# Kernel tuning notes

Hardware: AMD Instinct MI355X
Metric: run time of the kernel (lower is better)

Reference implementation:

```python
import jax, jax.numpy as jnp
import numpy as np

EMBED = 256
NH = 8
NL = 3
NP = 4
HD = EMBED // NH
P2 = 2 * NP  # left+right sampling points are concatenated along the point axis
SHAPES = [(100, 100), (50, 50), (25, 25)]


def setup_inputs() -> dict:
    key = jax.random.key(0)
    ks = jax.random.split(key, 10)
    b, nq, nk = 4, 300, 17
    lq = nq * nk
    L = sum(h * w for h, w in SHAPES)

    def lin(k, o, i):
        return jax.random.normal(k, (o, i), jnp.float32) / np.float32(np.sqrt(i))

    return {
        "query": jax.random.normal(ks[0], (b, lq, EMBED), jnp.float32),
        "reference_points_l": jax.random.uniform(ks[1], (b, nq, NL, nk, 2), jnp.float32),
        "reference_points_r": jax.random.uniform(ks[2], (b, nq, NL, nk, 2), jnp.float32),
        "value": jax.random.normal(ks[3], (b, L, EMBED * 2), jnp.float32),
        "value_spatial_shapes": jnp.array(SHAPES, jnp.int32),
        "value_mask": jnp.zeros((b, L), bool),
        "W_off": lin(ks[4], NH * NL * NP * 4, EMBED),
        "b_off": jax.random.normal(ks[5], (NH * NL * NP * 4,), jnp.float32) * 0.01,
        "W_attn": lin(ks[6], NH * NL * NP, EMBED),
        "b_attn": jnp.zeros((NH * NL * NP,), jnp.float32),
        "W_val": lin(ks[7], EMBED, EMBED * 2),
        "b_val": jnp.zeros((EMBED,), jnp.float32),
        "W_out": lin(ks[8], EMBED, EMBED),
        "b_out": jnp.zeros((EMBED,), jnp.float32),
    }


def _bilinear_sample(v_flat, locs, H, W):
    # v_flat: [b, nh, H*W, hd]; locs: [b, nh, lq, P, 2] normalized to [0,1].
    # Matches torch grid_sample(bilinear, padding=zeros, align_corners=False)
    # with grid = 2*loc - 1  =>  pixel coord = loc*size - 0.5.
    x = locs[..., 0] * W - 0.5
    y = locs[..., 1] * H - 0.5
    x0 = jnp.floor(x)
    y0 = jnp.floor(y)
    tx = x - x0
    ty = y - y0
    x0i = x0.astype(jnp.int32)
    y0i = y0.astype(jnp.int32)
    b, nh, lq, P = x.shape
    out = jnp.zeros(x.shape + (v_flat.shape[-1],), v_flat.dtype)
    for dy, wy in ((0, 1.0 - ty), (1, ty)):
        for dx, wx in ((0, 1.0 - tx), (1, tx)):
            xi = x0i + dx
            yi = y0i + dy
            valid = (xi >= 0) & (xi < W) & (yi >= 0) & (yi < H)
            idx = jnp.clip(yi, 0, H - 1) * W + jnp.clip(xi, 0, W - 1)
            g = jnp.take_along_axis(
                v_flat, idx.reshape(b, nh, lq * P, 1), axis=2
            ).reshape(b, nh, lq, P, -1)
            out = out + (wx * wy * valid.astype(v_flat.dtype))[..., None] * g
    return out


def reference(query, reference_points_l, reference_points_r, value,
              value_spatial_shapes, value_mask,
              W_off, b_off, W_attn, b_attn, W_val, b_val, W_out, b_out):
    shapes = np.asarray(value_spatial_shapes)  # static level shapes
    b, lq, _ = query.shape

    # value projection + padding mask (True -> zero, matching masked_fill)
    v = value @ W_val.T + b_val
    v = jnp.where(value_mask[..., None], jnp.zeros((), v.dtype), v)
    v = v.reshape(b, -1, NH, HD)

    off = (query @ W_off.T + b_off).reshape(b, lq, NH, NL, NP, 4)
    aw = (query @ W_attn.T + b_attn).reshape(b, lq, NH, NL * NP)
    aw = jax.nn.softmax(aw, axis=-1).reshape(b, lq, NH, NL, NP)

    # rearrange 'b nq nl nk s -> b (nq nk) nl s'
    rl = jnp.transpose(reference_points_l, (0, 1, 3, 2, 4)).reshape(b, lq, NL, 2)
    rr = jnp.transpose(reference_points_r, (0, 1, 3, 2, 4)).reshape(b, lq, NL, 2)

    # offset normalizer: (W, H) per level
    norm = jnp.stack([value_spatial_shapes[:, 1], value_spatial_shapes[:, 0]], -1).astype(query.dtype)
    locs_l = rl[:, :, None, :, None, :] + off[..., :2] / norm[None, None, None, :, None, :]
    locs_r = rr[:, :, None, :, None, :] + off[..., 2:] / norm[None, None, None, :, None, :]
    locs = jnp.concatenate([locs_l, locs_r], axis=-2)  # [b,lq,nh,nl,P2,2]
    w = jnp.concatenate([aw, aw], axis=-1)             # [b,lq,nh,nl,P2]

    out = jnp.zeros((b, NH, lq, HD), query.dtype)
    start = 0
    for l in range(NL):
        H, W = int(shapes[l, 0]), int(shapes[l, 1])
        v_l = jnp.transpose(v[:, start:start + H * W], (0, 2, 1, 3))  # [b,nh,HW,hd]
        locs_lvl = jnp.transpose(locs[:, :, :, l], (0, 2, 1, 3, 4))   # [b,nh,lq,P2,2]
        samp = _bilinear_sample(v_l, locs_lvl, H, W)                  # [b,nh,lq,P2,hd]
        w_lvl = jnp.transpose(w[:, :, :, l], (0, 2, 1, 3))            # [b,nh,lq,P2]
        out = out + jnp.einsum('bnqp,bnqpd->bnqd', w_lvl, samp)
        start += H * W

    out = jnp.transpose(out, (0, 2, 1, 3)).reshape(b, lq, EMBED)
    return out @ W_out.T + b_out
```

## Files before the change

### kernel.cpp

```cpp
#include <hip/hip_runtime.h>

#define NH    8
#define NLVL  3
#define HD    32
#define EMBED 256

constexpr int LTOT = 13125;
constexpr int BQ   = 4;
constexpr int NQ   = 300;
constexpr int NK   = 17;
constexpr int LQ   = NQ * NK;
constexpr int MV   = BQ * LTOT;
constexpr int MQ   = BQ * LQ;

typedef _Float16 f16x8 __attribute__((ext_vector_type(8)));
typedef _Float16 f16x4 __attribute__((ext_vector_type(4)));
typedef float    f32x4 __attribute__((ext_vector_type(4)));

constexpr int CW_WV   = 32768;
constexpr int CW_WOFF = CW_WV   + 24576;
constexpr int CW_WAT  = CW_WOFF + 6144;
constexpr int CW_TOT  = CW_WAT  + 16384;

__global__ __launch_bounds__(256)
void convert_w(const float* __restrict__ Wval, const float* __restrict__ Woff,
               const float* __restrict__ Wattn, const float* __restrict__ Wout,
               const float* __restrict__ boff, const float* __restrict__ battn,
               _Float16* __restrict__ Wv16, _Float16* __restrict__ Wqc16,
               _Float16* __restrict__ Wo16, float* __restrict__ bqc)
{
    const int idx = blockIdx.x * 256 + threadIdx.x;
    if (idx < 480) bqc[idx] = (idx < 384) ? boff[idx] : battn[idx - 384];
    if (idx >= CW_TOT) return;

    const float* src; _Float16* dst; size_t e;
    if      (idx < CW_WV)   { src = Wval;  dst = Wv16;          e = (size_t)idx * 4; }
    else if (idx < CW_WOFF) { src = Woff;  dst = Wqc16;         e = (size_t)(idx - CW_WV) * 4; }
    else if (idx < CW_WAT)  { src = Wattn; dst = Wqc16 + 98304; e = (size_t)(idx - CW_WOFF) * 4; }
    else                    { src = Wout;  dst = Wo16;          e = (size_t)(idx - CW_WAT) * 4; }

    const float4 x = *reinterpret_cast<const float4*>(src + e);
    f16x4 o;
    o[0] = (_Float16)x.x; o[1] = (_Float16)x.y;
    o[2] = (_Float16)x.z; o[3] = (_Float16)x.w;
    *reinterpret_cast<f16x4*>(dst + e) = o;
}

template<bool AF16, int OUT>
__global__ __launch_bounds__(256)
void gemm_f16(const float* __restrict__ A32, const _Float16* __restrict__ A16,
              const _Float16* __restrict__ Bg,
              const float* __restrict__ bias,
              float* __restrict__ Cf, _Float16* __restrict__ Ch,
              int M, int N, int K, const unsigned char* __restrict__ rowmask)
{
    __shared__ _Float16 Ah[2][4096], Bh[2][4096];

    const int tid  = threadIdx.x;
    const int lane = tid & 63;
    const int w    = tid >> 6;
    const int wr   = w >> 1, wc = w & 1;
    const int row0 = blockIdx.y * 128;
    const int col0 = blockIdx.x * 128;
    const int nt   = K >> 5;

    int cr[2], ck[2];
#pragma unroll
    for (int s = 0; s < 2; ++s) {
        const int i = tid + s * 256;
        cr[s] = ((i >> 6) << 4) + (i & 15);
        ck[s] = ((i >> 4) & 3) << 3;
    }

    float4 a32r[2][2];
    uint4  a16r[2], bhr[2];

    auto issue = [&](int kt) {
        const int kk = kt << 5;
#pragma unroll
        for (int s = 0; s < 2; ++s) {
            const int ga = row0 + cr[s];
            const size_t ao = (size_t)ga * K + kk + ck[s];
            if constexpr (AF16) {
                if (ga < M) a16r[s] = *reinterpret_cast<const uint4*>(A16 + ao);
                else        a16r[s] = make_uint4(0, 0, 0, 0);
            } else {
                if (ga < M) {
                    a32r[s][0] = *reinterpret_cast<const float4*>(A32 + ao);
                    a32r[s][1] = *reinterpret_cast<const float4*>(A32 + ao + 4);
                } else {
                    a32r[s][0] = make_float4(0.f, 0.f, 0.f, 0.f);
                    a32r[s][1] = make_float4(0.f, 0.f, 0.f, 0.f);
                }
            }
            const int gb = col0 + cr[s];
            if (gb < N)
                bhr[s] = *reinterpret_cast<const uint4*>(Bg + (size_t)gb * K + kk + ck[s]);
            else
                bhr[s] = make_uint4(0, 0, 0, 0);
        }
    };
    auto commit = [&](int buf) {
#pragma unroll
        for (int s = 0; s < 2; ++s) {
            const int i = tid + s * 256;
            if constexpr (AF16) {
                *reinterpret_cast<uint4*>(&Ah[buf][i * 8]) = a16r[s];
            } else {
                float x[8] = {a32r[s][0].x, a32r[s][0].y, a32r[s][0].z, a32r[s][0].w,
                              a32r[s][1].x, a32r[s][1].y, a32r[s][1].z, a32r[s][1].w};
                f16x8 h;
#pragma unroll
                for (int e = 0; e < 8; ++e) h[e] = (_Float16)x[e];
                ((f16x8*)Ah[buf])[i] = h;
            }
            *reinterpret_cast<uint4*>(&Bh[buf][i * 8]) = bhr[s];
        }
    };

    f32x4 acc[4][4];
#pragma unroll
    for (int i = 0; i < 4; ++i)
#pragma unroll
        for (int j = 0; j < 4; ++j) acc[i][j] = (f32x4)(0.f);

    issue(0);
    commit(0);
    __syncthreads();

    int cur = 0;
    for (int t = 0; t < nt; ++t) {
        const bool more = (t + 1 < nt);
        if (more) issue(t + 1);

        f16x8 af[4], bf[4];
#pragma unroll
        for (int ii = 0; ii < 4; ++ii) {
            af[ii] = ((f16x8*)Ah[cur])[(wr * 4 + ii) * 64 + lane];
            bf[ii] = ((f16x8*)Bh[cur])[(wc * 4 + ii) * 64 + lane];
        }
#pragma unroll
        for (int ii = 0; ii < 4; ++ii)
#pragma unroll
            for (int jj = 0; jj < 4; ++jj)
                acc[ii][jj] = __builtin_amdgcn_mfma_f32_16x16x32_f16(af[ii], bf[jj], acc[ii][jj], 0, 0, 0);

        if (more) {
            commit(cur ^ 1);
            __syncthreads();
        }
        cur ^= 1;
    }

    const int rbase = row0 + wr * 64 + (lane >> 4) * 4;
    const int cbase = col0 + wc * 64 + (lane & 15);
#pragma unroll
    for (int jj = 0; jj < 4; ++jj) {
        const int col = cbase + jj * 16;
        if (col >= N) continue;
        const float bv = bias[col];
#pragma unroll
        for (int ii = 0; ii < 4; ++ii)
#pragma unroll
            for (int r4 = 0; r4 < 4; ++r4) {
                const int row = rbase + ii * 16 + r4;
                if (row >= M) continue;
                float val = acc[ii][jj][r4] + bv;
                if constexpr (OUT == 1) {
                    if (rowmask[row]) val = 0.f;
                    const unsigned br = (unsigned)row / 13125u;
                    const int      lr = row - (int)br * 13125;
                    const int      hh = col >> 5, ch = col & 31;
                    Ch[(((size_t)br * NH + hh) * LTOT + lr) * 32 + ch] = (_Float16)val;
                } else if constexpr (OUT == 2) {
                    Ch[(size_t)row * N + col] = (_Float16)val;
                } else {
                    Cf[(size_t)row * N + col] = val;
                }
            }
    }
}

__global__ __launch_bounds__(256)
void msda_sample(const _Float16* __restrict__ v,
                 const _Float16* __restrict__ qo,
                 const float* __restrict__ refl,
                 const float* __restrict__ refr,
                 _Float16* __restrict__ out_pre)
{
    const int g   = threadIdx.x >> 6;
    const int t   = threadIdx.x & 63;
    const int bq  = blockIdx.x * 4 + g;
    const int b   = bq / LQ;
    const int lqi = bq - b * LQ;
    const int iq  = lqi / NK;
    const int ik  = lqi - iq * NK;

    __shared__ float s_off[4][384];
    __shared__ float s_aw[4][96];
    __shared__ float s_ref[4][NLVL][4];

    {
        const _Float16* qop = qo + (size_t)bq * 480;
        for (int i = t; i < 384; i += 64) s_off[g][i] = (float)qop[i];
        for (int i = t; i < 96;  i += 64) s_aw[g][i]  = (float)qop[384 + i];
        if (t < 12) {
            const int nl = t >> 2, comp = t & 3;
            const float* rp = (comp < 2) ? refl : refr;
            s_ref[g][nl][comp] =
                rp[((((size_t)b * NQ + iq) * NLVL + nl) * NK + ik) * 2 + (comp & 1)];
        }
    }
    __syncthreads();

    const int h  = t >> 3;
    const int c4 = (t & 7) * 4;

    float w12[12];
    float mx = -1e30f;
#pragma unroll
    for (int i = 0; i < 12; ++i) { w12[i] = s_aw[g][h * 12 + i]; mx = fmaxf(mx, w12[i]); }
    float sum = 0.f;
#pragma unroll
    for (int i = 0; i < 12; ++i) { w12[i] = __expf(w12[i] - mx); sum += w12[i]; }
    const float inv = 1.f / sum;

    const int   Ls[3]   = {100, 50, 25};
    const int   st[3]   = {0, 10000, 12500};
    const float invN[3] = {0.01f, 0.02f, 0.04f};

    float4 acc = make_float4(0.f, 0.f, 0.f, 0.f);
    const _Float16* vb = v + ((size_t)(b * NH + h) * LTOT) * 32 + c4;

#pragma unroll
    for (int nl = 0; nl < 3; ++nl) {
        const int   Wl = Ls[nl], Hl = Ls[nl];
        const float fS = (float)Wl;
        const int   base = st[nl];
#pragma unroll
        for (int p2 = 0; p2 < 8; ++p2) {
            const int p  = p2 & 3;
            const int rs = (p2 >> 2) & 1;
            const int ob = ((h * 3 + nl) * 4 + p) * 4 + rs * 2;
            const float ox = s_off[g][ob], oy = s_off[g][ob + 1];
            const float rx = s_ref[g][nl][rs * 2], ry = s_ref[g][nl][rs * 2 + 1];
            const float x = (rx + ox * invN[nl]) * fS - 0.5f;
            const float y = (ry + oy * invN[nl]) * fS - 0.5f;
            const float x0 = floorf(x), y0 = floorf(y);
            const float tx = x - x0,   ty = y - y0;
            const int ix = (int)x0, iy = (int)y0;
            const float aww = w12[nl * 4 + p] * inv;

            const int x0c = min(max(ix, 0), Wl - 1);
            const int x1c = min(max(ix + 1, 0), Wl - 1);
            const int y0c = min(max(iy, 0), Hl - 1);
            const int y1c = min(max(iy + 1, 0), Hl - 1);
            const float vx0 = (ix     >= 0 && ix     < Wl) ? 1.f : 0.f;
            const float vx1 = (ix + 1 >= 0 && ix + 1 < Wl) ? 1.f : 0.f;
            const float vy0 = (iy     >= 0 && iy     < Hl) ? 1.f : 0.f;
            const float vy1 = (iy + 1 >= 0 && iy + 1 < Hl) ? 1.f : 0.f;

            const float w00 = (1.f - tx) * (1.f - ty) * vx0 * vy0 * aww;
            const float w10 = tx         * (1.f - ty) * vx1 * vy0 * aww;
            const float w01 = (1.f - tx) * ty         * vx0 * vy1 * aww;
            const float w11 = tx         * ty         * vx1 * vy1 * aww;

            const f16x4 g00 = *reinterpret_cast<const f16x4*>(vb + (size_t)(base + y0c * Wl + x0c) * 32);
            const f16x4 g10 = *reinterpret_cast<const f16x4*>(vb + (size_t)(base + y0c * Wl + x1c) * 32);
            const f16x4 g01 = *reinterpret_cast<const f16x4*>(vb + (size_t)(base + y1c * Wl + x0c) * 32);
            const f16x4 g11 = *reinterpret_cast<const f16x4*>(vb + (size_t)(base + y1c * Wl + x1c) * 32);

            acc.x = fmaf(w00, (float)g00[0], fmaf(w10, (float)g10[0], fmaf(w01, (float)g01[0], fmaf(w11, (float)g11[0], acc.x))));
            acc.y = fmaf(w00, (float)g00[1], fmaf(w10, (float)g10[1], fmaf(w01, (float)g01[1], fmaf(w11, (float)g11[1], acc.y))));
            acc.z = fmaf(w00, (float)g00[2], fmaf(w10, (float)g10[2], fmaf(w01, (float)g01[2], fmaf(w11, (float)g11[2], acc.z))));
            acc.w = fmaf(w00, (float)g00[3], fmaf(w10, (float)g10[3], fmaf(w01, (float)g01[3], fmaf(w11, (float)g11[3], acc.w))));
        }
    }

    f16x4 o;
    o[0] = (_Float16)acc.x; o[1] = (_Float16)acc.y;
    o[2] = (_Float16)acc.z; o[3] = (_Float16)acc.w;
    *reinterpret_cast<f16x4*>(out_pre + (size_t)bq * EMBED + h * HD + c4) = o;
}

extern "C" void kernel_launch(void* const* d_in, const int* in_sizes, int n_in,
                              void* d_out, int out_size, void* d_ws, size_t ws_size,
                              hipStream_t stream)
{
    const float* query  = (const float*)d_in[0];
    const float* refl   = (const float*)d_in[1];
    const float* refr   = (const float*)d_in[2];
    const float* value  = (const float*)d_in[3];
    const unsigned char* vmask = (const unsigned char*)d_in[5];
    const float* W_off  = (const float*)d_in[6];
    const float* b_off  = (const float*)d_in[7];
    const float* W_attn = (const float*)d_in[8];
    const float* b_attn = (const float*)d_in[9];
    const float* W_val  = (const float*)d_in[10];
    const float* b_val  = (const float*)d_in[11];
    const float* W_out  = (const float*)d_in[12];
    const float* b_out  = (const float*)d_in[13];

    char* p = (char*)d_ws;
    _Float16* v      = (_Float16*)p;  p += (size_t)MV * 256 * 2;
    _Float16* qo     = (_Float16*)p;  p += (size_t)MQ * 480 * 2;
    _Float16* outp   = (_Float16*)p;  p += (size_t)MQ * 256 * 2;
    _Float16* Wv16   = (_Float16*)p;  p += 131072 * 2;
    _Float16* Wqc16  = (_Float16*)p;  p += 122880 * 2;
    _Float16* Wo16   = (_Float16*)p;  p += 65536 * 2;
    float* bqc       = (float*)p;     p += 480 * 4;

    convert_w<<<dim3((CW_TOT + 255) / 256), 256, 0, stream>>>(
        W_val, W_off, W_attn, W_out, b_off, b_attn, Wv16, Wqc16, Wo16, bqc);

    gemm_f16<false, 1><<<dim3(2, (MV + 127) / 128), 256, 0, stream>>>(
        value, nullptr, Wv16, b_val, nullptr, v, MV, 256, 512, vmask);

    gemm_f16<false, 2><<<dim3(4, (MQ + 127) / 128), 256, 0, stream>>>(
        query, nullptr, Wqc16, bqc, nullptr, qo, MQ, 480, 256, nullptr);

    msda_sample<<<dim3(MQ / 4), 256, 0, stream>>>(v, qo, refl, refr, outp);

    gemm_f16<true, 0><<<dim3(2, (MQ + 127) / 128), 256, 0, stream>>>(
        nullptr, outp, Wo16, b_out, (float*)d_out, nullptr, MQ, 256, 256, nullptr);
}
```

Baseline: 383.0 us.

## Fuse value/query GEMMs, remap sampler blocks per XCD, precompute sampling metadata

Merges the value and query projection GEMMs into one launch and changes both GEMM kernels to 512-thread blocks where each wave holds a smaller accumulator tile. The sampling kernel maps blocks so each batch's work lands on a fixed pair of XCDs, improving L2 reuse of that batch's value tensor. It also computes the softmax and bilinear corner indices and weights once per point cooperatively into shared memory, instead of redundantly in every thread. The cost is extra shared memory and barriers in the sampler, plus idle padding blocks.

```diff
diff --git a/kernel.cpp b/kernel.cpp
--- a/kernel.cpp
+++ b/kernel.cpp
@@ -12,6 +12,10 @@
 constexpr int LQ   = NQ * NK;
 constexpr int MV   = BQ * LTOT;
 constexpr int MQ   = BQ * LQ;
+
+constexpr int NBLK_V  = 822;
+constexpr int NBLK_QC = 640;
+constexpr int QBPB    = 1275;
 
 typedef _Float16 f16x8 __attribute__((ext_vector_type(8)));
 typedef _Float16 f16x4 __attribute__((ext_vector_type(4)));
@@ -46,13 +50,12 @@
     *reinterpret_cast<f16x4*>(dst + e) = o;
 }
 
-template<bool AF16, int OUT>
-__global__ __launch_bounds__(256)
-void gemm_f16(const float* __restrict__ A32, const _Float16* __restrict__ A16,
-              const _Float16* __restrict__ Bg,
-              const float* __restrict__ bias,
-              float* __restrict__ Cf, _Float16* __restrict__ Ch,
-              int M, int N, int K, const unsigned char* __restrict__ rowmask)
+__global__ __launch_bounds__(512)
+void gemm_vq(const float* __restrict__ value, const _Float16* __restrict__ Wv,
+             const float* __restrict__ bval, _Float16* __restrict__ vout,
+             const unsigned char* __restrict__ vmask,
+             const float* __restrict__ query, const _Float16* __restrict__ Wqc,
+             const float* __restrict__ bqcv, _Float16* __restrict__ qo)
 {
     __shared__ _Float16 Ah[2][4096], Bh[2][4096];
 
@@ -60,67 +63,58 @@
     const int lane = tid & 63;
     const int w    = tid >> 6;
     const int wr   = w >> 1, wc = w & 1;
-    const int row0 = blockIdx.y * 128;
-    const int col0 = blockIdx.x * 128;
-    const int nt   = K >> 5;
-
-    int cr[2], ck[2];
-#pragma unroll
-    for (int s = 0; s < 2; ++s) {
-        const int i = tid + s * 256;
-        cr[s] = ((i >> 6) << 4) + (i & 15);
-        ck[s] = ((i >> 4) & 3) << 3;
-    }
-
-    float4 a32r[2][2];
-    uint4  a16r[2], bhr[2];
+
+    const int  bid = blockIdx.x;
+    const bool isV = bid < NBLK_V;
+    const float* A; const _Float16* Bg; const float* bias;
+    int M, N, K, row0, col0;
+    if (isV) {
+        A = value; Bg = Wv; bias = bval;
+        M = MV; N = 256; K = 512;
+        col0 = (bid & 1) << 7; row0 = (bid >> 1) << 7;
+    } else {
+        const int b2 = bid - NBLK_V;
+        A = query; Bg = Wqc; bias = bqcv;
+        M = MQ; N = 480; K = 256;
+        col0 = (b2 & 3) << 7; row0 = (b2 >> 2) << 7;
+    }
+    const int nt = K >> 5;
+
+    const int cr = ((tid >> 6) << 4) + (tid & 15);
+    const int ck = ((tid >> 4) & 3) << 3;
+
+    float4 a0, a1; uint4 brg;
 
     auto issue = [&](int kt) {
         const int kk = kt << 5;
-#pragma unroll
-        for (int s = 0; s < 2; ++s) {
-            const int ga = row0 + cr[s];
-            const size_t ao = (size_t)ga * K + kk + ck[s];
-            if constexpr (AF16) {
-                if (ga < M) a16r[s] = *reinterpret_cast<const uint4*>(A16 + ao);
-                else        a16r[s] = make_uint4(0, 0, 0, 0);
-            } else {
-                if (ga < M) {
-                    a32r[s][0] = *reinterpret_cast<const float4*>(A32 + ao);
-                    a32r[s][1] = *reinterpret_cast<const float4*>(A32 + ao + 4);
-                } else {
-                    a32r[s][0] = make_float4(0.f, 0.f, 0.f, 0.f);
-                    a32r[s][1] = make_float4(0.f, 0.f, 0.f, 0.f);
-                }
-            }
-            const int gb = col0 + cr[s];
-            if (gb < N)
-                bhr[s] = *reinterpret_cast<const uint4*>(Bg + (size_t)gb * K + kk + ck[s]);
-            else
-                bhr[s] = make_uint4(0, 0, 0, 0);
+        const int ga = row0 + cr;
+        if (ga < M) {
+            const float* ap = A + (size_t)ga * K + kk + ck;
+            a0 = *reinterpret_cast<const float4*>(ap);
+            a1 = *reinterpret_cast<const float4*>(ap + 4);
+        } else {
+            a0 = make_float4(0.f, 0.f, 0.f, 0.f);
+            a1 = make_float4(0.f, 0.f, 0.f, 0.f);
         }
+        const int gb = col0 + cr;
+        if (gb < N)
+            brg = *reinterpret_cast<const uint4*>(Bg + (size_t)gb * K + kk + ck);
+        else
+            brg = make_uint4(0, 0, 0, 0);
     };
     auto commit = [&](int buf) {
-#pragma unroll
-        for (int s = 0; s < 2; ++s) {
-            const int i = tid + s * 256;
-            if constexpr (AF16) {
-                *reinterpret_cast<uint4*>(&Ah[buf][i * 8]) = a16r[s];
-            } else {
-                float x[8] = {a32r[s][0].x, a32r[s][0].y, a32r[s][0].z, a32r[s][0].w,
-                              a32r[s][1].x, a32r[s][1].y, a32r[s][1].z, a32r[s][1].w};
-                f16x8 h;
-#pragma unroll
-                for (int e = 0; e < 8; ++e) h[e] = (_Float16)x[e];
-                ((f16x8*)Ah[buf])[i] = h;
-            }
-            *reinterpret_cast<uint4*>(&Bh[buf][i * 8]) = bhr[s];
-        }
+        f16x8 h;
+        h[0] = (_Float16)a0.x; h[1] = (_Float16)a0.y;
+        h[2] = (_Float16)a0.z; h[3] = (_Float16)a0.w;
+        h[4] = (_Float16)a1.x; h[5] = (_Float16)a1.y;
+        h[6] = (_Float16)a1.z; h[7] = (_Float16)a1.w;
+        ((f16x8*)Ah[buf])[tid] = h;
+        *reinterpret_cast<uint4*>(&Bh[buf][tid * 8]) = brg;
     };
 
-    f32x4 acc[4][4];
-#pragma unroll
-    for (int i = 0; i < 4; ++i)
+    f32x4 acc[2][4];
+#pragma unroll
+    for (int i = 0; i < 2; ++i)
 #pragma unroll
         for (int j = 0; j < 4; ++j) acc[i][j] = (f32x4)(0.f);
 
@@ -133,14 +127,16 @@
         const bool more = (t + 1 < nt);
         if (more) issue(t + 1);
 
-        f16x8 af[4], bf[4];
-#pragma unroll
-        for (int ii = 0; ii < 4; ++ii) {
-            af[ii] = ((f16x8*)Ah[cur])[(wr * 4 + ii) * 64 + lane];
-            bf[ii] = ((f16x8*)Bh[cur])[(wc * 4 + ii) * 64 + lane];
-        }
-#pragma unroll
-        for (int ii = 0; ii < 4; ++ii)
+        f16x8 af[2], bf[4];
+#pragma unroll
+        for (int ii = 0; ii < 2; ++ii)
+            af[ii] = ((f16x8*)Ah[cur])[(wr * 2 + ii) * 64 + lane];
+#pragma unroll
+        for (int jj = 0; jj < 4; ++jj)
+            bf[jj] = ((f16x8*)Bh[cur])[(wc * 4 + jj) * 64 + lane];
+
+#pragma unroll
+        for (int ii = 0; ii < 2; ++ii)
 #pragma unroll
             for (int jj = 0; jj < 4; ++jj)
                 acc[ii][jj] = __builtin_amdgcn_mfma_f32_16x16x32_f16(af[ii], bf[jj], acc[ii][jj], 0, 0, 0);
@@ -152,7 +148,7 @@
         cur ^= 1;
     }
 
-    const int rbase = row0 + wr * 64 + (lane >> 4) * 4;
+    const int rbase = row0 + wr * 32 + (lane >> 4) * 4;
     const int cbase = col0 + wc * 64 + (lane & 15);
 #pragma unroll
     for (int jj = 0; jj < 4; ++jj) {
@@ -160,23 +156,105 @@
         if (col >= N) continue;
         const float bv = bias[col];
 #pragma unroll
-        for (int ii = 0; ii < 4; ++ii)
+        for (int ii = 0; ii < 2; ++ii)
 #pragma unroll
             for (int r4 = 0; r4 < 4; ++r4) {
                 const int row = rbase + ii * 16 + r4;
                 if (row >= M) continue;
                 float val = acc[ii][jj][r4] + bv;
-                if constexpr (OUT == 1) {
-                    if (rowmask[row]) val = 0.f;
+                if (isV) {
+                    if (vmask[row]) val = 0.f;
                     const unsigned br = (unsigned)row / 13125u;
                     const int      lr = row - (int)br * 13125;
                     const int      hh = col >> 5, ch = col & 31;
-                    Ch[(((size_t)br * NH + hh) * LTOT + lr) * 32 + ch] = (_Float16)val;
-                } else if constexpr (OUT == 2) {
-                    Ch[(size_t)row * N + col] = (_Float16)val;
+                    vout[(((size_t)br * NH + hh) * LTOT + lr) * 32 + ch] = (_Float16)val;
                 } else {
-                    Cf[(size_t)row * N + col] = val;
+                    qo[(size_t)row * 480 + col] = (_Float16)val;
                 }
+            }
+    }
+}
+
+__global__ __launch_bounds__(512)
+void gemm_out(const _Float16* __restrict__ A, const _Float16* __restrict__ Bg,
+              const float* __restrict__ bias, float* __restrict__ C)
+{
+    __shared__ _Float16 Ah[2][4096], Bh[2][4096];
+
+    const int tid  = threadIdx.x;
+    const int lane = tid & 63;
+    const int w    = tid >> 6;
+    const int wr   = w >> 1, wc = w & 1;
+    const int bid  = blockIdx.x;
+    const int col0 = (bid & 1) << 7;
+    const int row0 = (bid >> 1) << 7;
+    constexpr int M = MQ, N = 256, K = 256, nt = K >> 5;
+
+    const int cr = ((tid >> 6) << 4) + (tid & 15);
+    const int ck = ((tid >> 4) & 3) << 3;
+
+    uint4 arg, brg;
+    auto issue = [&](int kt) {
+        const int kk = kt << 5;
+        const int ga = row0 + cr;
+        if (ga < M) arg = *reinterpret_cast<const uint4*>(A + (size_t)ga * K + kk + ck);
+        else        arg = make_uint4(0, 0, 0, 0);
+        brg = *reinterpret_cast<const uint4*>(Bg + (size_t)(col0 + cr) * K + kk + ck);
+    };
+    auto commit = [&](int buf) {
+        *reinterpret_cast<uint4*>(&Ah[buf][tid * 8]) = arg;
+        *reinterpret_cast<uint4*>(&Bh[buf][tid * 8]) = brg;
+    };
+
+    f32x4 acc[2][4];
+#pragma unroll
+    for (int i = 0; i < 2; ++i)
+#pragma unroll
+        for (int j = 0; j < 4; ++j) acc[i][j] = (f32x4)(0.f);
+
+    issue(0);
+    commit(0);
+    __syncthreads();
+
+    int cur = 0;
+    for (int t = 0; t < nt; ++t) {
+        const bool more = (t + 1 < nt);
+        if (more) issue(t + 1);
+
+        f16x8 af[2], bf[4];
+#pragma unroll
+        for (int ii = 0; ii < 2; ++ii)
+            af[ii] = ((f16x8*)Ah[cur])[(wr * 2 + ii) * 64 + lane];
+#pragma unroll
+        for (int jj = 0; jj < 4; ++jj)
+            bf[jj] = ((f16x8*)Bh[cur])[(wc * 4 + jj) * 64 + lane];
+
+#pragma unroll
+        for (int ii = 0; ii < 2; ++ii)
+#pragma unroll
+            for (int jj = 0; jj < 4; ++jj)
+                acc[ii][jj] = __builtin_amdgcn_mfma_f32_16x16x32_f16(af[ii], bf[jj], acc[ii][jj], 0, 0, 0);
+
+        if (more) {
+            commit(cur ^ 1);
+            __syncthreads();
+        }
+        cur ^= 1;
+    }
+
+    const int rbase = row0 + wr * 32 + (lane >> 4) * 4;
+    const int cbase = col0 + wc * 64 + (lane & 15);
+#pragma unroll
+    for (int jj = 0; jj < 4; ++jj) {
+        const int col = cbase + jj * 16;
+        const float bv = bias[col];
+#pragma unroll
+        for (int ii = 0; ii < 2; ++ii)
+#pragma unroll
+            for (int r4 = 0; r4 < 4; ++r4) {
+                const int row = rbase + ii * 16 + r4;
+                if (row >= M) continue;
+                C[(size_t)row * N + col] = acc[ii][jj][r4] + bv;
             }
     }
 }
@@ -188,17 +266,25 @@
                  const float* __restrict__ refr,
                  _Float16* __restrict__ out_pre)
 {
+    const int bid = blockIdx.x;
+    const int xcd = bid & 7;
+    const int k   = xcd >> 1;
+    const int j   = ((bid >> 3) << 1) | (xcd & 1);
+    if (j >= QBPB) return;
+
     const int g   = threadIdx.x >> 6;
     const int t   = threadIdx.x & 63;
-    const int bq  = blockIdx.x * 4 + g;
-    const int b   = bq / LQ;
-    const int lqi = bq - b * LQ;
+    const int b   = k;
+    const int lqi = j * 4 + g;
+    const int bq  = b * LQ + lqi;
     const int iq  = lqi / NK;
     const int ik  = lqi - iq * NK;
 
     __shared__ float s_off[4][384];
     __shared__ float s_aw[4][96];
     __shared__ float s_ref[4][NLVL][4];
+    __shared__ int   s_idx[4][192][4];
+    __shared__ float s_w[4][192][4];
 
     {
         const _Float16* qop = qo + (size_t)bq * 480;
@@ -213,68 +299,84 @@
     }
     __syncthreads();
 
+    if (t < 8) {
+        float mx = -1e30f;
+#pragma unroll
+        for (int i = 0; i < 12; ++i) mx = fmaxf(mx, s_aw[g][t * 12 + i]);
+        float sum = 0.f;
+        float e[12];
+#pragma unroll
+        for (int i = 0; i < 12; ++i) { e[i] = __expf(s_aw[g][t * 12 + i] - mx); sum += e[i]; }
+        const float inv = 1.f / sum;
+#pragma unroll
+        for (int i = 0; i < 12; ++i) s_aw[g][t * 12 + i] = e[i] * inv;
+    }
+    __syncthreads();
+
+#pragma unroll
+    for (int kk = 0; kk < 3; ++kk) {
+        const int tau = kk * 64 + t;
+        const int pt = tau >> 3, h = tau & 7;
+        const int nl = pt >> 3, p2 = pt & 7, p = p2 & 3, rs = p2 >> 2;
+        const int   Wl   = 100 >> nl;
+        const int   base = (nl == 0) ? 0 : ((nl == 1) ? 10000 : 12500);
+        const float invN = 0.01f * (float)(1 << nl);
+        const float fS   = (float)Wl;
+
+        const int ob = ((h * 3 + nl) * 4 + p) * 4 + rs * 2;
+        const float ox = s_off[g][ob], oy = s_off[g][ob + 1];
+        const float rx = s_ref[g][nl][rs * 2], ry = s_ref[g][nl][rs * 2 + 1];
+        const float x = (rx + ox * invN) * fS - 0.5f;
+        const float y = (ry + oy * invN) * fS - 0.5f;
+        const float x0f = floorf(x), y0f = floorf(y);
+        const float tx = x - x0f, ty = y - y0f;
+        const int ix = (int)x0f, iy = (int)y0f;
+        const float aww = s_aw[g][h * 12 + nl * 4 + p];
+
+        const int x0c = min(max(ix, 0), Wl - 1);
+        const int x1c = min(max(ix + 1, 0), Wl - 1);
+        const int y0c = min(max(iy, 0), Wl - 1);
+        const int y1c = min(max(iy + 1, 0), Wl - 1);
+        const float vx0 = (ix     >= 0 && ix     < Wl) ? 1.f : 0.f;
+        const float vx1 = (ix + 1 >= 0 && ix + 1 < Wl) ? 1.f : 0.f;
+        const float vy0 = (iy     >= 0 && iy     < Wl) ? 1.f : 0.f;
+        const float vy1 = (iy + 1 >= 0 && iy + 1 < Wl) ? 1.f : 0.f;
+
+        int4 idx;
+        idx.x = (base + y0c * Wl + x0c) * 32;
+        idx.y = (base + y0c * Wl + x1c) * 32;
+        idx.z = (base + y1c * Wl + x0c) * 32;
+        idx.w = (base + y1c * Wl + x1c) * 32;
+        float4 wv;
+        wv.x = (1.f - tx) * (1.f - ty) * vx0 * vy0 * aww;
+        wv.y = tx         * (1.f - ty) * vx1 * vy0 * aww;
+        wv.z = (1.f - tx) * ty         * vx0 * vy1 * aww;
+        wv.w = tx         * ty         * vx1 * vy1 * aww;
+
+        *reinterpret_cast<int4*>(&s_idx[g][tau][0]) = idx;
+        *reinterpret_cast<float4*>(&s_w[g][tau][0]) = wv;
+    }
+    __syncthreads();
+
     const int h  = t >> 3;
     const int c4 = (t & 7) * 4;
-
-    float w12[12];
-    float mx = -1e30f;
-#pragma unroll
-    for (int i = 0; i < 12; ++i) { w12[i] = s_aw[g][h * 12 + i]; mx = fmaxf(mx, w12[i]); }
-    float sum = 0.f;
-#pragma unroll
-    for (int i = 0; i < 12; ++i) { w12[i] = __expf(w12[i] - mx); sum += w12[i]; }
-    const float inv = 1.f / sum;
-
-    const int   Ls[3]   = {100, 50, 25};
-    const int   st[3]   = {0, 10000, 12500};
-    const float invN[3] = {0.01f, 0.02f, 0.04f};
+    const _Float16* vh = v + ((size_t)(b * NH + h) * LTOT) * 32 + c4;
 
     float4 acc = make_float4(0.f, 0.f, 0.f, 0.f);
-    const _Float16* vb = v + ((size_t)(b * NH + h) * LTOT) * 32 + c4;
-
-#pragma unroll
-    for (int nl = 0; nl < 3; ++nl) {
-        const int   Wl = Ls[nl], Hl = Ls[nl];
-        const float fS = (float)Wl;
-        const int   base = st[nl];
-#pragma unroll
-        for (int p2 = 0; p2 < 8; ++p2) {
-            const int p  = p2 & 3;
-            const int rs = (p2 >> 2) & 1;
-            const int ob = ((h * 3 + nl) * 4 + p) * 4 + rs * 2;
-            const float ox = s_off[g][ob], oy = s_off[g][ob + 1];
-            const float rx = s_ref[g][nl][rs * 2], ry = s_ref[g][nl][rs * 2 + 1];
-            const float x = (rx + ox * invN[nl]) * fS - 0.5f;
-            const float y = (ry + oy * invN[nl]) * fS - 0.5f;
-            const float x0 = floorf(x), y0 = floorf(y);
-            const float tx = x - x0,   ty = y - y0;
-            const int ix = (int)x0, iy = (int)y0;
-            const float aww = w12[nl * 4 + p] * inv;
-
-            const int x0c = min(max(ix, 0), Wl - 1);
-            const int x1c = min(max(ix + 1, 0), Wl - 1);
-            const int y0c = min(max(iy, 0), Hl - 1);
-            const int y1c = min(max(iy + 1, 0), Hl - 1);
-            const float vx0 = (ix     >= 0 && ix     < Wl) ? 1.f : 0.f;
-            const float vx1 = (ix + 1 >= 0 && ix + 1 < Wl) ? 1.f : 0.f;
-            const float vy0 = (iy     >= 0 && iy     < Hl) ? 1.f : 0.f;
-            const float vy1 = (iy + 1 >= 0 && iy + 1 < Hl) ? 1.f : 0.f;
-
-            const float w00 = (1.f - tx) * (1.f - ty) * vx0 * vy0 * aww;
-            const float w10 = tx         * (1.f - ty) * vx1 * vy0 * aww;
-            const float w01 = (1.f - tx) * ty         * vx0 * vy1 * aww;
-            const float w11 = tx         * ty         * vx1 * vy1 * aww;
-
-            const f16x4 g00 = *reinterpret_cast<const f16x4*>(vb + (size_t)(base + y0c * Wl + x0c) * 32);
-            const f16x4 g10 = *reinterpret_cast<const f16x4*>(vb + (size_t)(base + y0c * Wl + x1c) * 32);
-            const f16x4 g01 = *reinterpret_cast<const f16x4*>(vb + (size_t)(base + y1c * Wl + x0c) * 32);
-            const f16x4 g11 = *reinterpret_cast<const f16x4*>(vb + (size_t)(base + y1c * Wl + x1c) * 32);
-
-            acc.x = fmaf(w00, (float)g00[0], fmaf(w10, (float)g10[0], fmaf(w01, (float)g01[0], fmaf(w11, (float)g11[0], acc.x))));
-            acc.y = fmaf(w00, (float)g00[1], fmaf(w10, (float)g10[1], fmaf(w01, (float)g01[1], fmaf(w11, (float)g11[1], acc.y))));
-            acc.z = fmaf(w00, (float)g00[2], fmaf(w10, (float)g10[2], fmaf(w01, (float)g01[2], fmaf(w11, (float)g11[2], acc.z))));
-            acc.w = fmaf(w00, (float)g00[3], fmaf(w10, (float)g10[3], fmaf(w01, (float)g01[3], fmaf(w11, (float)g11[3], acc.w))));
-        }
+#pragma unroll
+    for (int pt = 0; pt < 24; ++pt) {
+        const int tau = pt * 8 + h;
+        const int4   idx = *reinterpret_cast<const int4*>(&s_idx[g][tau][0]);
+        const float4 wv  = *reinterpret_cast<const float4*>(&s_w[g][tau][0]);
+        const f16x4 g00 = *reinterpret_cast<const f16x4*>(vh + idx.x);
+        const f16x4 g10 = *reinterpret_cast<const f16x4*>(vh + idx.y);
+        const f16x4 g01 = *reinterpret_cast<const f16x4*>(vh + idx.z);
+        const f16x4 g11 = *reinterpret_cast<const f16x4*>(vh + idx.w);
+
+        acc.x = fmaf(wv.x, (float)g00[0], fmaf(wv.y, (float)g10[0], fmaf(wv.z, (float)g01[0], fmaf(wv.w, (float)g11[0], acc.x))));
+        acc.y = fmaf(wv.x, (float)g00[1], fmaf(wv.y, (float)g10[1], fmaf(wv.z, (float)g01[1], fmaf(wv.w, (float)g11[1], acc.y))));
+        acc.z = fmaf(wv.x, (float)g00[2], fmaf(wv.y, (float)g10[2], fmaf(wv.z, (float)g01[2], fmaf(wv.w, (float)g11[2], acc.z))));
+        acc.w = fmaf(wv.x, (float)g00[3], fmaf(wv.y, (float)g10[3], fmaf(wv.z, (float)g01[3], fmaf(wv.w, (float)g11[3], acc.w))));
     }
 
     f16x4 o;
@@ -313,14 +415,10 @@
     convert_w<<<dim3((CW_TOT + 255) / 256), 256, 0, stream>>>(
         W_val, W_off, W_attn, W_out, b_off, b_attn, Wv16, Wqc16, Wo16, bqc);
 
-    gemm_f16<false, 1><<<dim3(2, (MV + 127) / 128), 256, 0, stream>>>(
-        value, nullptr, Wv16, b_val, nullptr, v, MV, 256, 512, vmask);
-
-    gemm_f16<false, 2><<<dim3(4, (MQ + 127) / 128), 256, 0, stream>>>(
-        query, nullptr, Wqc16, bqc, nullptr, qo, MQ, 480, 256, nullptr);
-
-    msda_sample<<<dim3(MQ / 4), 256, 0, stream>>>(v, qo, refl, refr, outp);
-
-    gemm_f16<true, 0><<<dim3(2, (MQ + 127) / 128), 256, 0, stream>>>(
-        nullptr, outp, Wo16, b_out, (float*)d_out, nullptr, MQ, 256, 256, nullptr);
+    gemm_vq<<<dim3(NBLK_V + NBLK_QC), 512, 0, stream>>>(
+        value, Wv16, b_val, v, vmask, query, Wqc16, bqc, qo);
+
+    msda_sample<<<dim3(5103), 256, 0, stream>>>(v, qo, refl, refr, outp);
+
+    gemm_out<<<dim3(320), 512, 0, stream>>>(outp, Wo16, b_out, (float*)d_out);
 }
```

Result: faster. 344.3 us (-10.1%).
